# Optimization experiments

Hardware: AMD Instinct MI355X
Metric: run time of the kernel (lower is better)

The kernel has to match this reference:

```python
import jax, jax.numpy as jnp
import numpy as np

TEMPERATURE = 0.02
B, S, D_TOK, H = 128, 32, 128, 128  # batch, query tokens, doc tokens, hidden dim


def setup_inputs() -> dict:
    key = jax.random.key(0)
    kq, kp = jax.random.split(key)
    query_embeddings = jax.random.normal(kq, (B, S, H), dtype=jnp.float32)
    positive_embeddings = jax.random.normal(kp, (B, D_TOK, H), dtype=jnp.float32)
    return {"query_embeddings": query_embeddings, "positive_embeddings": positive_embeddings}


def reference(query_embeddings, positive_embeddings):
    # Late interaction: [b, c, s, d] = every query token vs every doc token (in-batch negatives)
    late = jnp.einsum('bsh,cdh->bcsd', query_embeddings, positive_embeddings)
    # MaxSim over doc tokens, sum over query tokens -> [b, c] score matrix
    scores = late.max(axis=-1).sum(axis=-1) / TEMPERATURE
    # In-batch negatives: label for row i is column i (the diagonal is the positive)
    logp = jax.nn.log_softmax(scores, axis=-1)
    loss = -jnp.mean(jnp.diagonal(logp))
    return loss
```

## Files before the change

kernel.cpp:

```cpp
#include <hip/hip_runtime.h>
#include <hip/hip_bf16.h>

typedef __bf16 bf16x8 __attribute__((ext_vector_type(8)));
typedef __bf16 bf16x4 __attribute__((ext_vector_type(4)));
typedef float  f32x4  __attribute__((ext_vector_type(4)));

#define P_CHUNKS (128 * 128 * 16)
#define Q_CHUNKS (128 * 32 * 16)
#define WS_NEED  ((size_t)(P_CHUNKS + Q_CHUNKS) * 16 + 128 * 128 * 4 + 4)

__global__ __launch_bounds__(256) void convert_kernel(
    const float* __restrict__ Q, const float* __restrict__ P,
    unsigned short* __restrict__ wp, unsigned short* __restrict__ wq)
{
    const int g = blockIdx.x * 256 + threadIdx.x;
    const float* src;
    unsigned short* dst;
    if (g < P_CHUNKS) {
        const int c = g >> 11, rem = g & 2047;
        const int dj = rem >> 8, k = (rem >> 6) & 3, l = rem & 63;
        src = P + ((size_t)c << 14) + (dj * 16 + (l & 15)) * 128 + k * 32 + (l >> 4) * 8;
        dst = wp + ((size_t)g << 3);
    } else {
        const int g2 = g - P_CHUNKS;
        const int b = g2 >> 9, j = g2 & 511;
        const int si = j >> 8, k = (j >> 6) & 3, l = j & 63;
        src = Q + (size_t)b * 4096 + (si * 16 + (l & 15)) * 128 + k * 32 + (l >> 4) * 8;
        dst = wq + ((size_t)g2 << 3);
    }
    float4 v0 = *(const float4*)src;
    float4 v1 = *(const float4*)(src + 4);
    bf16x8 o = { (__bf16)v0.x, (__bf16)v0.y, (__bf16)v0.z, (__bf16)v0.w,
                 (__bf16)v1.x, (__bf16)v1.y, (__bf16)v1.z, (__bf16)v1.w };
    *(bf16x8*)dst = o;
}

__global__ __launch_bounds__(256, 2) void colbert_scores_reg(
    const unsigned short* __restrict__ Pb,
    const unsigned short* __restrict__ Qb,
    float* __restrict__ scores)
{
    const int tid  = threadIdx.x;
    const int lane = tid & 63;
    const int wave = tid >> 6;

    const int xcd = blockIdx.x & 7;
    const int i   = blockIdx.x >> 3;
    const int c   = (xcd << 4) + (i & 15);
    const int qtr = i >> 4;

    const unsigned short* pw = Pb + ((size_t)c << 14);
    bf16x8 bp[8][4];
    #pragma unroll
    for (int dj = 0; dj < 8; dj++)
        #pragma unroll
        for (int k = 0; k < 4; k++)
            bp[dj][k] = *(const bf16x8*)(pw + (((dj << 2) + k) << 9) + (lane << 3));

    #pragma unroll 1
    for (int it = 0; it < 8; it++) {
        const int b = (qtr << 5) + (wave << 3) + it;
        const unsigned short* qw = Qb + ((size_t)b << 12);

        bf16x8 aq[2][4];
        #pragma unroll
        for (int k = 0; k < 4; k++) {
            aq[0][k] = *(const bf16x8*)(qw + (k << 9) + (lane << 3));
            aq[1][k] = *(const bf16x8*)(qw + 2048 + (k << 9) + (lane << 3));
        }

        float m0[4] = {-1e30f, -1e30f, -1e30f, -1e30f};
        float m1[4] = {-1e30f, -1e30f, -1e30f, -1e30f};
        #pragma unroll
        for (int dj = 0; dj < 8; dj++) {
            f32x4 t0 = (f32x4){0.f, 0.f, 0.f, 0.f};
            f32x4 t1 = (f32x4){0.f, 0.f, 0.f, 0.f};
            #pragma unroll
            for (int k = 0; k < 4; k++) {
                t0 = __builtin_amdgcn_mfma_f32_16x16x32_bf16(aq[0][k], bp[dj][k], t0, 0, 0, 0);
                t1 = __builtin_amdgcn_mfma_f32_16x16x32_bf16(aq[1][k], bp[dj][k], t1, 0, 0, 0);
            }
            #pragma unroll
            for (int r = 0; r < 4; r++) {
                m0[r] = fmaxf(m0[r], t0[r]);
                m1[r] = fmaxf(m1[r], t1[r]);
            }
        }

        float partial = 0.f;
        #pragma unroll
        for (int r = 0; r < 4; r++) {
            float v = m0[r];
            v = fmaxf(v, __shfl_xor(v, 1)); v = fmaxf(v, __shfl_xor(v, 2));
            v = fmaxf(v, __shfl_xor(v, 4)); v = fmaxf(v, __shfl_xor(v, 8));
            partial += v;
            float w = m1[r];
            w = fmaxf(w, __shfl_xor(w, 1)); w = fmaxf(w, __shfl_xor(w, 2));
            w = fmaxf(w, __shfl_xor(w, 4)); w = fmaxf(w, __shfl_xor(w, 8));
            partial += w;
        }
        partial += __shfl_xor(partial, 16);
        partial += __shfl_xor(partial, 32);
        if (lane == 0) scores[b * 128 + c] = partial * 50.0f;
    }
}

__global__ __launch_bounds__(1024) void colbert_loss_kernel(
    const float* __restrict__ scores, unsigned* __restrict__ out)
{
    __shared__ float wpart[16];
    const int lane = threadIdx.x & 63;
    const int wave = threadIdx.x >> 6;
    float acc = 0.f;
    #pragma unroll
    for (int i = 0; i < 8; i++) {
        const int r = wave + (i << 4);
        const float* row = scores + r * 128;
        float v0 = row[lane], v1 = row[lane + 64];
        float mx = fmaxf(v0, v1);
        mx = fmaxf(mx, __shfl_xor(mx, 1));  mx = fmaxf(mx, __shfl_xor(mx, 2));
        mx = fmaxf(mx, __shfl_xor(mx, 4));  mx = fmaxf(mx, __shfl_xor(mx, 8));
        mx = fmaxf(mx, __shfl_xor(mx, 16)); mx = fmaxf(mx, __shfl_xor(mx, 32));
        float e = expf(v0 - mx) + expf(v1 - mx);
        e += __shfl_xor(e, 1);  e += __shfl_xor(e, 2);  e += __shfl_xor(e, 4);
        e += __shfl_xor(e, 8);  e += __shfl_xor(e, 16); e += __shfl_xor(e, 32);
        float diag = (r < 64) ? __shfl(v0, r) : __shfl(v1, r - 64);
        acc += diag - (mx + logf(e));
    }
    if (lane == 0) wpart[wave] = acc;
    __syncthreads();
    if (threadIdx.x == 0) {
        float t = 0.f;
        #pragma unroll
        for (int i = 0; i < 16; i++) t += wpart[i];
        float loss = -t / 128.0f;
        unsigned bits = __float_as_uint(loss);
        unsigned rnd  = (bits + 0x7FFFu + ((bits >> 16) & 1u)) & 0xFFFF0000u;
        out[0] = rnd | (rnd >> 16);
    }
}

__global__ __launch_bounds__(256, 2) void colbert_scores_slow(
    const float* __restrict__ Q, const float* __restrict__ P, float* __restrict__ scores)
{
    __shared__ __align__(16) unsigned short qs[4 * 32 * 128];
    __shared__ __align__(16) unsigned short ps[128 * 128];
    const int tid = threadIdx.x;
    const int b0 = (blockIdx.x & 31) * 4, c0 = (blockIdx.x >> 5) * 4;
    const float4* gq = (const float4*)(Q + (size_t)b0 * 4096);
    #pragma unroll
    for (int j = tid; j < 4096; j += 256) {
        float4 v = gq[j];
        int f = j << 2, row = f >> 7, h = f & 127;
        int dst = (row << 7) + (((h >> 3) ^ (row & 15)) << 3) + (h & 7);
        bf16x4 o = { (__bf16)v.x, (__bf16)v.y, (__bf16)v.z, (__bf16)v.w };
        *(bf16x4*)&qs[dst] = o;
    }
    const int lane = tid & 63, wave = tid >> 6, n = lane & 15, quad = lane >> 4;
    const unsigned short* qb = qs + wave * 4096;
    #pragma unroll 1
    for (int it = 0; it < 4; it++) {
        const int c = c0 + it;
        if (it) __syncthreads();
        const float4* gp = (const float4*)(P + (size_t)c * 16384);
        #pragma unroll
        for (int j = tid; j < 4096; j += 256) {
            float4 v = gp[j];
            int f = j << 2, d = f >> 7, h = f & 127;
            int dst = (d << 7) + (((h >> 3) ^ (d & 15)) << 3) + (h & 7);
            bf16x4 o = { (__bf16)v.x, (__bf16)v.y, (__bf16)v.z, (__bf16)v.w };
            *(bf16x4*)&ps[dst] = o;
        }
        __syncthreads();
        f32x4 acc[2][8];
        #pragma unroll
        for (int si = 0; si < 2; si++)
            #pragma unroll
            for (int dj = 0; dj < 8; dj++) acc[si][dj] = (f32x4){0.f,0.f,0.f,0.f};
        #pragma unroll
        for (int k = 0; k < 4; k++) {
            const int chunk = (((k << 2) + quad) ^ n) << 3;
            bf16x8 a0 = *(const bf16x8*)&qb[(n << 7) + chunk];
            bf16x8 a1 = *(const bf16x8*)&qb[((n + 16) << 7) + chunk];
            #pragma unroll
            for (int dj = 0; dj < 8; dj++) {
                bf16x8 bb = *(const bf16x8*)&ps[((dj * 16 + n) << 7) + chunk];
                acc[0][dj] = __builtin_amdgcn_mfma_f32_16x16x32_bf16(a0, bb, acc[0][dj], 0, 0, 0);
                acc[1][dj] = __builtin_amdgcn_mfma_f32_16x16x32_bf16(a1, bb, acc[1][dj], 0, 0, 0);
            }
        }
        float partial = 0.f;
        #pragma unroll
        for (int si = 0; si < 2; si++)
            #pragma unroll
            for (int r = 0; r < 4; r++) {
                float m = acc[si][0][r];
                #pragma unroll
                for (int dj = 1; dj < 8; dj++) m = fmaxf(m, acc[si][dj][r]);
                m = fmaxf(m, __shfl_xor(m, 1)); m = fmaxf(m, __shfl_xor(m, 2));
                m = fmaxf(m, __shfl_xor(m, 4)); m = fmaxf(m, __shfl_xor(m, 8));
                partial += m;
            }
        partial += __shfl_xor(partial, 16);
        partial += __shfl_xor(partial, 32);
        if (lane == 0) scores[(b0 + wave) * 128 + c] = partial * 50.0f;
    }
}

extern "C" void kernel_launch(void* const* d_in, const int* in_sizes, int n_in,
                              void* d_out, int out_size, void* d_ws, size_t ws_size,
                              hipStream_t stream) {
    const float* Q = (const float*)d_in[0];
    const float* P = (const float*)d_in[1];

    if (ws_size >= WS_NEED) {
        unsigned short* wp = (unsigned short*)d_ws;
        unsigned short* wq = wp + (size_t)P_CHUNKS * 8;
        float* scores = (float*)(wq + (size_t)Q_CHUNKS * 8);
        convert_kernel<<<dim3((P_CHUNKS + Q_CHUNKS) / 256), dim3(256), 0, stream>>>(
            Q, P, wp, wq);
        colbert_scores_reg<<<dim3(512), dim3(256), 0, stream>>>(wp, wq, scores);
        colbert_loss_kernel<<<dim3(1), dim3(1024), 0, stream>>>(scores, (unsigned*)d_out);
    } else {
        float* scores = (float*)d_ws;
        colbert_scores_slow<<<dim3(1024), dim3(256), 0, stream>>>(Q, P, scores);
        colbert_loss_kernel<<<dim3(1), dim3(1024), 0, stream>>>(scores, (unsigned*)d_out);
    }
}
```

Baseline: 88.32 us.

## Fuse bf16 conversion into score kernel, drop separate convert pass

Removes the standalone fp32-to-bf16 convert kernel and its workspace round trip. The score kernel now reads fp32 Q and P straight from global memory in MFMA fragment order and converts them in registers. This saves one kernel launch and the write and re-read of the bf16 copies. In exchange, each block reads twice as many bytes per fragment, the loads are strided rather than contiguous, and Q tiles are converted again in every block that uses them. The shared-memory fallback path is also deleted.

Result: slower. 113.7 us (+28.7%).

```diff
diff --git a/kernel.cpp b/kernel.cpp
--- a/kernel.cpp
+++ b/kernel.cpp
@@ -2,42 +2,11 @@
 #include <hip/hip_bf16.h>
 
 typedef __bf16 bf16x8 __attribute__((ext_vector_type(8)));
-typedef __bf16 bf16x4 __attribute__((ext_vector_type(4)));
 typedef float  f32x4  __attribute__((ext_vector_type(4)));
 
-#define P_CHUNKS (128 * 128 * 16)
-#define Q_CHUNKS (128 * 32 * 16)
-#define WS_NEED  ((size_t)(P_CHUNKS + Q_CHUNKS) * 16 + 128 * 128 * 4 + 4)
-
-__global__ __launch_bounds__(256) void convert_kernel(
-    const float* __restrict__ Q, const float* __restrict__ P,
-    unsigned short* __restrict__ wp, unsigned short* __restrict__ wq)
-{
-    const int g = blockIdx.x * 256 + threadIdx.x;
-    const float* src;
-    unsigned short* dst;
-    if (g < P_CHUNKS) {
-        const int c = g >> 11, rem = g & 2047;
-        const int dj = rem >> 8, k = (rem >> 6) & 3, l = rem & 63;
-        src = P + ((size_t)c << 14) + (dj * 16 + (l & 15)) * 128 + k * 32 + (l >> 4) * 8;
-        dst = wp + ((size_t)g << 3);
-    } else {
-        const int g2 = g - P_CHUNKS;
-        const int b = g2 >> 9, j = g2 & 511;
-        const int si = j >> 8, k = (j >> 6) & 3, l = j & 63;
-        src = Q + (size_t)b * 4096 + (si * 16 + (l & 15)) * 128 + k * 32 + (l >> 4) * 8;
-        dst = wq + ((size_t)g2 << 3);
-    }
-    float4 v0 = *(const float4*)src;
-    float4 v1 = *(const float4*)(src + 4);
-    bf16x8 o = { (__bf16)v0.x, (__bf16)v0.y, (__bf16)v0.z, (__bf16)v0.w,
-                 (__bf16)v1.x, (__bf16)v1.y, (__bf16)v1.z, (__bf16)v1.w };
-    *(bf16x8*)dst = o;
-}
-
-__global__ __launch_bounds__(256, 2) void colbert_scores_reg(
-    const unsigned short* __restrict__ Pb,
-    const unsigned short* __restrict__ Qb,
+__global__ __launch_bounds__(256, 2) void colbert_scores_f32(
+    const float* __restrict__ Q,
+    const float* __restrict__ P,
     float* __restrict__ scores)
 {
     const int tid  = threadIdx.x;
@@ -49,24 +18,39 @@
     const int c   = (xcd << 4) + (i & 15);
     const int qtr = i >> 4;
 
-    const unsigned short* pw = Pb + ((size_t)c << 14);
+    const int row_a = lane & 15;
+    const int ko8   = (lane >> 4) * 8;
+
+    const float* pw = P + ((size_t)c << 14);
     bf16x8 bp[8][4];
     #pragma unroll
-    for (int dj = 0; dj < 8; dj++)
+    for (int dj = 0; dj < 8; dj++) {
         #pragma unroll
-        for (int k = 0; k < 4; k++)
-            bp[dj][k] = *(const bf16x8*)(pw + (((dj << 2) + k) << 9) + (lane << 3));
+        for (int k = 0; k < 4; k++) {
+            const float* s = pw + (dj * 16 + row_a) * 128 + k * 32 + ko8;
+            float4 v0 = *(const float4*)s;
+            float4 v1 = *(const float4*)(s + 4);
+            bp[dj][k] = (bf16x8){ (__bf16)v0.x, (__bf16)v0.y, (__bf16)v0.z, (__bf16)v0.w,
+                                  (__bf16)v1.x, (__bf16)v1.y, (__bf16)v1.z, (__bf16)v1.w };
+        }
+    }
 
     #pragma unroll 1
     for (int it = 0; it < 8; it++) {
         const int b = (qtr << 5) + (wave << 3) + it;
-        const unsigned short* qw = Qb + ((size_t)b << 12);
+        const float* qw = Q + ((size_t)b << 12);
 
         bf16x8 aq[2][4];
         #pragma unroll
-        for (int k = 0; k < 4; k++) {
-            aq[0][k] = *(const bf16x8*)(qw + (k << 9) + (lane << 3));
-            aq[1][k] = *(const bf16x8*)(qw + 2048 + (k << 9) + (lane << 3));
+        for (int si = 0; si < 2; si++) {
+            #pragma unroll
+            for (int k = 0; k < 4; k++) {
+                const float* s = qw + (si * 16 + row_a) * 128 + k * 32 + ko8;
+                float4 v0 = *(const float4*)s;
+                float4 v1 = *(const float4*)(s + 4);
+                aq[si][k] = (bf16x8){ (__bf16)v0.x, (__bf16)v0.y, (__bf16)v0.z, (__bf16)v0.w,
+                                      (__bf16)v1.x, (__bf16)v1.y, (__bf16)v1.z, (__bf16)v1.w };
+            }
         }
 
         float m0[4] = {-1e30f, -1e30f, -1e30f, -1e30f};
@@ -140,90 +124,13 @@
     }
 }
 
-__global__ __launch_bounds__(256, 2) void colbert_scores_slow(
-    const float* __restrict__ Q, const float* __restrict__ P, float* __restrict__ scores)
-{
-    __shared__ __align__(16) unsigned short qs[4 * 32 * 128];
-    __shared__ __align__(16) unsigned short ps[128 * 128];
-    const int tid = threadIdx.x;
-    const int b0 = (blockIdx.x & 31) * 4, c0 = (blockIdx.x >> 5) * 4;
-    const float4* gq = (const float4*)(Q + (size_t)b0 * 4096);
-    #pragma unroll
-    for (int j = tid; j < 4096; j += 256) {
-        float4 v = gq[j];
-        int f = j << 2, row = f >> 7, h = f & 127;
-        int dst = (row << 7) + (((h >> 3) ^ (row & 15)) << 3) + (h & 7);
-        bf16x4 o = { (__bf16)v.x, (__bf16)v.y, (__bf16)v.z, (__bf16)v.w };
-        *(bf16x4*)&qs[dst] = o;
-    }
-    const int lane = tid & 63, wave = tid >> 6, n = lane & 15, quad = lane >> 4;
-    const unsigned short* qb = qs + wave * 4096;
-    #pragma unroll 1
-    for (int it = 0; it < 4; it++) {
-        const int c = c0 + it;
-        if (it) __syncthreads();
-        const float4* gp = (const float4*)(P + (size_t)c * 16384);
-        #pragma unroll
-        for (int j = tid; j < 4096; j += 256) {
-            float4 v = gp[j];
-            int f = j << 2, d = f >> 7, h = f & 127;
-            int dst = (d << 7) + (((h >> 3) ^ (d & 15)) << 3) + (h & 7);
-            bf16x4 o = { (__bf16)v.x, (__bf16)v.y, (__bf16)v.z, (__bf16)v.w };
-            *(bf16x4*)&ps[dst] = o;
-        }
-        __syncthreads();
-        f32x4 acc[2][8];
-        #pragma unroll
-        for (int si = 0; si < 2; si++)
-            #pragma unroll
-            for (int dj = 0; dj < 8; dj++) acc[si][dj] = (f32x4){0.f,0.f,0.f,0.f};
-        #pragma unroll
-        for (int k = 0; k < 4; k++) {
-            const int chunk = (((k << 2) + quad) ^ n) << 3;
-            bf16x8 a0 = *(const bf16x8*)&qb[(n << 7) + chunk];
-            bf16x8 a1 = *(const bf16x8*)&qb[((n + 16) << 7) + chunk];
-            #pragma unroll
-            for (int dj = 0; dj < 8; dj++) {
-                bf16x8 bb = *(const bf16x8*)&ps[((dj * 16 + n) << 7) + chunk];
-                acc[0][dj] = __builtin_amdgcn_mfma_f32_16x16x32_bf16(a0, bb, acc[0][dj], 0, 0, 0);
-                acc[1][dj] = __builtin_amdgcn_mfma_f32_16x16x32_bf16(a1, bb, acc[1][dj], 0, 0, 0);
-            }
-        }
-        float partial = 0.f;
-        #pragma unroll
-        for (int si = 0; si < 2; si++)
-            #pragma unroll
-            for (int r = 0; r < 4; r++) {
-                float m = acc[si][0][r];
-                #pragma unroll
-                for (int dj = 1; dj < 8; dj++) m = fmaxf(m, acc[si][dj][r]);
-                m = fmaxf(m, __shfl_xor(m, 1)); m = fmaxf(m, __shfl_xor(m, 2));
-                m = fmaxf(m, __shfl_xor(m, 4)); m = fmaxf(m, __shfl_xor(m, 8));
-                partial += m;
-            }
-        partial += __shfl_xor(partial, 16);
-        partial += __shfl_xor(partial, 32);
-        if (lane == 0) scores[(b0 + wave) * 128 + c] = partial * 50.0f;
-    }
-}
-
 extern "C" void kernel_launch(void* const* d_in, const int* in_sizes, int n_in,
                               void* d_out, int out_size, void* d_ws, size_t ws_size,
                               hipStream_t stream) {
     const float* Q = (const float*)d_in[0];
     const float* P = (const float*)d_in[1];
+    float* scores  = (float*)d_ws;
 
-    if (ws_size >= WS_NEED) {
-        unsigned short* wp = (unsigned short*)d_ws;
-        unsigned short* wq = wp + (size_t)P_CHUNKS * 8;
-        float* scores = (float*)(wq + (size_t)Q_CHUNKS * 8);
-        convert_kernel<<<dim3((P_CHUNKS + Q_CHUNKS) / 256), dim3(256), 0, stream>>>(
-            Q, P, wp, wq);
-        colbert_scores_reg<<<dim3(512), dim3(256), 0, stream>>>(wp, wq, scores);
-        colbert_loss_kernel<<<dim3(1), dim3(1024), 0, stream>>>(scores, (unsigned*)d_out);
-    } else {
-        float* scores = (float*)d_ws;
-        colbert_scores_slow<<<dim3(1024), dim3(256), 0, stream>>>(Q, P, scores);
-        colbert_loss_kernel<<<dim3(1), dim3(1024), 0, stream>>>(scores, (unsigned*)d_out);
-    }
+    colbert_scores_f32<<<dim3(512), dim3(256), 0, stream>>>(Q, P, scores);
+    colbert_loss_kernel<<<dim3(1), dim3(1024), 0, stream>>>(scores, (unsigned*)d_out);
 }
```
